# Performance work log

Hardware: AMD Instinct MI355X
Metric: run time of the kernel (lower is better)

## Reference

```python
import jax, jax.numpy as jnp
import numpy as np

E = 1024   # embed_dim
H = 512    # hidden_dim
LD = 512   # latent_dim
B = 2048   # number of users / segments
L = 48     # max segment length (pad target)


def _lrelu(x):
    return jnp.where(x > 0, x, 0.2 * x)


def setup_inputs() -> dict:
    key = jax.random.key(0)
    ks = list(jax.random.split(key, 40))
    nxt = iter(ks)

    def nrm(shape, s=1.0):
        return (jax.random.normal(next(nxt), shape, jnp.float32) * s).astype(jnp.float32)

    # ragged segment boundaries: lengths cycle {16..48}, mean 32, total 65536
    pat = np.array([16, 20, 28, 32, 32, 36, 44, 48], dtype=np.int64)
    lens = np.tile(pat, B // 8)
    starts = np.concatenate([np.zeros(1, np.int64), np.cumsum(lens)[:-1]])
    N = int(lens.sum())  # 65536
    seq_start_end = jnp.asarray(np.stack([starts, starts + lens], axis=1))

    inp = {
        'target_chosen': nrm((B, E)),
        'target_rejected': nrm((B, E)),
        'context_chosen': nrm((N, E)),
        'context_rejected': nrm((N, E)),
        'eps': nrm((B, LD)),
        # PairEncoder: 2E -> H -> H -> LD
        'pe_w1': nrm((2 * E, H), 0.02), 'pe_b1': jnp.zeros((H,), jnp.float32),
        'pe_w2': nrm((H, H), 0.02),     'pe_b2': jnp.zeros((H,), jnp.float32),
        'pe_w3': nrm((H, LD), 0.02),    'pe_b3': jnp.zeros((LD,), jnp.float32),
        # SequenceEncoder attention projections (LD -> LD)
        'wq': nrm((LD, LD), 0.02), 'bq': jnp.zeros((LD,), jnp.float32),
        'wk': nrm((LD, LD), 0.02), 'bk': jnp.zeros((LD,), jnp.float32),
        'wv': nrm((LD, LD), 0.02), 'bv': jnp.zeros((LD,), jnp.float32),
        'wm': nrm((LD, LD), 0.02), 'bm': jnp.zeros((LD,), jnp.float32),
        'wlv': nrm((LD, LD), 0.02), 'blv': jnp.zeros((LD,), jnp.float32),
        # Decoder: (E+LD) -> H -> H -> 1 (shared for chosen/rejected)
        'd_w1': nrm((E + LD, H), 0.02), 'd_b1': jnp.zeros((H,), jnp.float32),
        'd_w2': nrm((H, H), 0.02),      'd_b2': jnp.zeros((H,), jnp.float32),
        'd_w3': nrm((H, 1), 0.02),      'd_b3': jnp.zeros((1,), jnp.float32),
        'seq_start_end': seq_start_end,
        'user_type': jax.random.randint(next(nxt), (B,), 0, 4, jnp.int64),
    }
    return inp


def reference(target_chosen, target_rejected, context_chosen, context_rejected, eps,
              pe_w1, pe_b1, pe_w2, pe_b2, pe_w3, pe_b3,
              wq, bq, wk, bk, wv, bv, wm, bm, wlv, blv,
              d_w1, d_b1, d_w2, d_b2, d_w3, d_b3,
              seq_start_end, user_type):
    N = context_chosen.shape[0]

    # ---- PairEncoder: concat(chosen, rejected) -> MLP -> [N, LD] ----
    x = jnp.concatenate([context_chosen, context_rejected], axis=1)
    h = _lrelu(x @ pe_w1 + pe_b1)
    h = _lrelu(h @ pe_w2 + pe_b2)
    pair_embed = h @ pe_w3 + pe_b3  # [N, LD]

    # ---- SequenceEncoder: ragged per-segment self-attention + mean pool ----
    starts = seq_start_end[:, 0]
    lens = seq_start_end[:, 1] - starts            # [B]
    pos = jnp.arange(L)
    idx = jnp.clip(starts[:, None] + pos[None, :], 0, N - 1)   # [B, L]
    mask = pos[None, :] < lens[:, None]                        # [B, L]
    ctx = pair_embed[idx]                                      # [B, L, LD]

    q = ctx @ wq + bq
    k = ctx @ wk + bk
    v = ctx @ wv + bv
    scores = jnp.einsum('bld,bmd->blm', q, k) / jnp.float32(np.sqrt(LD))
    scores = jnp.where(mask[:, None, :], scores, jnp.float32(-1e9))
    attn = jax.nn.softmax(scores, axis=-1)
    weighted = jnp.einsum('blm,bmd->bld', attn, v)             # [B, L, LD]
    # mean over valid query rows only (matches exact-segment torch mean)
    seg_out = jnp.sum(weighted * mask[..., None], axis=1) / lens[:, None].astype(jnp.float32)

    mean = seg_out @ wm + bm
    log_var = seg_out @ wlv + blv
    mean = jnp.clip(mean, -1.0, 1.0)
    log_var = jnp.clip(log_var, -1.0, 1.0)

    # ---- reparameterization (training path) + sphere normalization ----
    z = mean + jnp.exp(0.5 * log_var) * eps
    znorm = jnp.maximum(jnp.linalg.norm(z, axis=-1, keepdims=True), 1e-12)
    z = z / znorm * jnp.float32(np.sqrt(LD))

    # ---- Decoder (shared MLP) ----
    def dec(t):
        u = jnp.concatenate([t, z], axis=1)
        u = _lrelu(u @ d_w1 + d_b1)
        u = _lrelu(u @ d_w2 + d_b2)
        return u @ d_w3 + d_b3

    rc = dec(target_chosen)
    rr = dec(target_rejected)
    return (rc, rr, mean, log_var, z)
```

## Files before the change

### kernel.cpp

```cpp
#include <hip/hip_runtime.h>
#include <stdint.h>

typedef __bf16 bf16;
typedef __attribute__((ext_vector_type(8))) __bf16 bf16x8;
typedef __attribute__((ext_vector_type(4))) float f32x4;
typedef __attribute__((ext_vector_type(4))) unsigned int u32x4;

typedef __attribute__((address_space(1))) unsigned gas_u32;
typedef __attribute__((address_space(3))) unsigned las_u32;

__device__ __forceinline__ unsigned short f2b_bits(float f) {
    unsigned u = __builtin_bit_cast(unsigned, f);
    u += 0x7fffu + ((u >> 16) & 1u);
    return (unsigned short)(u >> 16);
}
__device__ __forceinline__ bf16 f2b(float f) { return __builtin_bit_cast(bf16, f2b_bits(f)); }
__device__ __forceinline__ float lo16f(unsigned u) { return __builtin_bit_cast(float, u << 16); }
__device__ __forceinline__ float hi16f(unsigned u) { return __builtin_bit_cast(float, u & 0xffff0000u); }

__device__ __forceinline__ void gl2lds16(const void* g, void* l) {
    __builtin_amdgcn_global_load_lds((gas_u32*)(uintptr_t)g, (las_u32*)(uintptr_t)l, 16, 0, 0);
}

#define BM 128
#define BN 128
#define BK 32

template<int AMODE, int ACT, int OMODE>
__global__ __launch_bounds__(256, 2)
void gemm_k(const void* __restrict__ Ap, const void* __restrict__ Ap2,
            const bf16* __restrict__ Bt, const float* __restrict__ bias,
            void* __restrict__ Op, void* __restrict__ Op2,
            int M, int N, int K, int lda)
{
    constexpr int ASZ = (AMODE == 1) ? (BM * BK * 2) : (BM * BK);
    __shared__ __align__(16) bf16 As[ASZ];
    __shared__ __align__(16) bf16 Bs[BN * BK];
    float* Asf = (float*)As;

    const int tid  = threadIdx.x;
    const int wave = tid >> 6;
    const int lane = tid & 63;
    const int quad = lane >> 4;
    const int l16  = lane & 15;
    const int bm0 = blockIdx.y * BM;
    const int bn0 = blockIdx.x * BN;
    const int wm0 = (wave >> 1) << 6;
    const int wn0 = (wave & 1) << 6;

    f32x4 acc[4][4];
#pragma unroll
    for (int a = 0; a < 4; a++)
#pragma unroll
        for (int c = 0; c < 4; c++) acc[a][c] = {0.f, 0.f, 0.f, 0.f};

    const bf16* aptr[2];
    const float* asrc0[4];
    const float* asrc1[4];
    if constexpr (AMODE == 1) {
#pragma unroll
        for (int j = 0; j < 4; j++) {
            const int s2 = j * 256 + tid;
            const int arow = s2 >> 3, kq = s2 & 7;
            const int kgrp = kq ^ (arow & 7);
            asrc0[j] = (const float*)Ap  + (size_t)(bm0 + arow) * 1024 + kgrp * 4;
            asrc1[j] = (const float*)Ap2 + (size_t)(bm0 + arow) * 1024 + kgrp * 4;
        }
    } else {
#pragma unroll
        for (int i = 0; i < 2; i++) {
            const int s = i * 256 + tid;
            const int arow = s >> 2, kp = s & 3;
            size_t rbase;
            if constexpr (AMODE == 2) rbase = (size_t)((const int*)Ap2)[bm0 + arow] * (size_t)lda;
            else                      rbase = (size_t)(bm0 + arow) * (size_t)lda;
            aptr[i] = (const bf16*)Ap + rbase + kp * 8;
        }
    }
    const bf16* bptr[2];
#pragma unroll
    for (int i = 0; i < 2; i++) {
        const int s = i * 256 + tid;
        const int brow = s >> 2, kp = s & 3;
        bptr[i] = Bt + (size_t)(bn0 + brow) * (size_t)K + kp * 8;
    }

    for (int k0 = 0; k0 < K; k0 += BK) {
        if constexpr (AMODE == 1) {
#pragma unroll
            for (int j = 0; j < 4; j++) {
                const float* src = (k0 < 1024) ? (asrc0[j] + k0) : (asrc1[j] + (k0 - 1024));
                gl2lds16(src, &Asf[(j * 256 + (wave << 6)) * 4]);
            }
        } else {
#pragma unroll
            for (int i = 0; i < 2; i++)
                gl2lds16(aptr[i] + k0, &As[(i * 256 + (wave << 6)) * 8]);
        }
#pragma unroll
        for (int i = 0; i < 2; i++)
            gl2lds16(bptr[i] + k0, &Bs[(i * 256 + (wave << 6)) * 8]);

        __syncthreads();

        bf16x8 af[4], bfr[4];
#pragma unroll
        for (int mt = 0; mt < 4; mt++) {
            if constexpr (AMODE == 1) {
                const int r = wm0 + mt * 16 + l16;
                const int rx = r & 7;
                const f32x4 v0 = *(const f32x4*)&Asf[r * 32 + ((2 * quad) ^ rx) * 4];
                const f32x4 v1 = *(const f32x4*)&Asf[r * 32 + ((2 * quad + 1) ^ rx) * 4];
                bf16x8 t;
#pragma unroll
                for (int e = 0; e < 4; e++) { t[e] = (bf16)v0[e]; t[4 + e] = (bf16)v1[e]; }
                af[mt] = t;
            } else {
                af[mt] = *(const bf16x8*)&As[(wm0 + mt * 16 + l16) * BK + quad * 8];
            }
        }
#pragma unroll
        for (int nt = 0; nt < 4; nt++)
            bfr[nt] = *(const bf16x8*)&Bs[(wn0 + nt * 16 + l16) * BK + quad * 8];
#pragma unroll
        for (int mt = 0; mt < 4; mt++)
#pragma unroll
            for (int nt = 0; nt < 4; nt++)
                acc[mt][nt] = __builtin_amdgcn_mfma_f32_16x16x32_bf16(af[mt], bfr[nt], acc[mt][nt], 0, 0, 0);

        __syncthreads();
    }

    float bv[4];
#pragma unroll
    for (int nt = 0; nt < 4; nt++) bv[nt] = bias ? bias[bn0 + wn0 + nt * 16 + l16] : 0.f;
#pragma unroll
    for (int mt = 0; mt < 4; mt++) {
#pragma unroll
        for (int nt = 0; nt < 4; nt++) {
#pragma unroll
            for (int r = 0; r < 4; r++) {
                float v = acc[mt][nt][r] + bv[nt];
                if constexpr (ACT == 1) v = (v > 0.f) ? v : 0.2f * v;
                if constexpr (ACT == 2) v = fminf(fmaxf(v, -1.f), 1.f);
                const int row = bm0 + wm0 + mt * 16 + quad * 4 + r;
                const int col = bn0 + wn0 + nt * 16 + l16;
                if constexpr (OMODE == 0) {
                    ((bf16*)Op)[(size_t)row * N + col] = f2b(v);
                } else {
                    if (col < 512) ((float*)Op)[(size_t)row * 512 + col] = v;
                    else           ((float*)Op2)[(size_t)row * 512 + col - 512] = v;
                }
            }
        }
    }
}

struct TP8 { const float* s[8]; bf16* d[8]; };

__global__ __launch_bounds__(256)
void transpose8_k(TP8 p)
{
    __shared__ float t[64][65];
    const float* __restrict__ src = p.s[blockIdx.z];
    bf16* __restrict__ dst = p.d[blockIdx.z];
    const int tx = threadIdx.x & 63, ty = threadIdx.x >> 6;
    const int k0 = blockIdx.x * 64, n0 = blockIdx.y * 64;
#pragma unroll
    for (int j = 0; j < 16; j++) {
        const int r = j * 4 + ty;
        t[r][tx] = src[(size_t)(k0 + r) * 512 + n0 + tx];
    }
    __syncthreads();
#pragma unroll
    for (int j = 0; j < 16; j++) {
        const int r = j * 4 + ty;
        dst[(size_t)(n0 + r) * 512 + k0 + tx] = f2b(t[tx][r]);
    }
}

__global__ __launch_bounds__(256)
void transpose_g_k(const float* __restrict__ src, bf16* __restrict__ dst, int K)
{
    __shared__ float t[64][65];
    const int tx = threadIdx.x & 63, ty = threadIdx.x >> 6;
    const int k0 = blockIdx.x * 64, n0 = blockIdx.y * 64;
#pragma unroll
    for (int j = 0; j < 16; j++) {
        const int r = j * 4 + ty;
        t[r][tx] = src[(size_t)(k0 + r) * 512 + n0 + tx];
    }
    __syncthreads();
#pragma unroll
    for (int j = 0; j < 16; j++) {
        const int r = j * 4 + ty;
        dst[(size_t)(n0 + r) * K + k0 + tx] = f2b(t[tx][r]);
    }
}

__global__ void prep_misc_k(const float* bq, const float* bk, const float* bv,
                            const float* bm, const float* blv,
                            float* bqkv, float* bml,
                            const int* sse, int* rowidx, int Nctx)
{
    const int i = blockIdx.x * 256 + threadIdx.x;
    if (i < 512) {
        bqkv[i] = bq[i]; bqkv[512 + i] = bk[i]; bqkv[1024 + i] = bv[i];
        bml[i] = bm[i];  bml[512 + i] = blv[i];
    }
    if (i < 98304) {
        const int b = i / 48, l = i - b * 48;
        int s = sse[2 * b] + l;
        s = (s < 0) ? 0 : ((s >= Nctx) ? (Nctx - 1) : s);
        rowidx[i] = s;
    }
}

__global__ __launch_bounds__(256, 2)
void attn_k(const bf16* __restrict__ qkv, const int* __restrict__ sse, bf16* __restrict__ seg)
{
    __shared__ bf16 qsh[48 * 128];
    __shared__ bf16 ksh[48 * 128];
    __shared__ float ss[48 * 49];
    __shared__ float wbuf[4 * 48];
    __shared__ float wfin[48];

    const int b = blockIdx.x;
    const int tid = threadIdx.x;
    const int wave = tid >> 6, lane = tid & 63;
    const int len = sse[2 * b + 1] - sse[2 * b];
    const size_t rowbase = (size_t)b * (48 * 1536);

    int pl[9], pm[9]; float sc[9];
    const int np = len * len;
#pragma unroll
    for (int i = 0; i < 9; i++) {
        const int p = tid + i * 256;
        if (p < np) { pl[i] = p / len; pm[i] = p - pl[i] * len; }
        else pl[i] = -1;
        sc[i] = 0.f;
    }

    int srow[3], scol[3];
#pragma unroll
    for (int j = 0; j < 3; j++) { const int t = j * 256 + tid; srow[j] = t >> 4; scol[j] = t & 15; }

    for (int ch = 0; ch < 4; ch++) {
#pragma unroll
        for (int j = 0; j < 3; j++) {
            const int row = srow[j], c = scol[j];
            const bf16* g = qkv + rowbase + (size_t)row * 1536 + (ch << 7) + (c << 3);
            const int lc = row * 128 + ((c ^ (row & 15)) << 3);
            *(bf16x8*)&qsh[lc] = *(const bf16x8*)g;
            *(bf16x8*)&ksh[lc] = *(const bf16x8*)(g + 512);
        }
        __syncthreads();
#pragma unroll
        for (int i = 0; i < 9; i++) {
            if (pl[i] < 0) continue;
            const int l = pl[i], m = pm[i];
            const int lbase = l * 128, mbase = m * 128;
            const int lx = l & 15, mx = m & 15;
            float s0 = 0.f, s1 = 0.f;
#pragma unroll 1
            for (int c8 = 0; c8 < 16; c8++) {
                const bf16x8 qv = *(const bf16x8*)&qsh[lbase + ((c8 ^ lx) << 3)];
                const bf16x8 kv = *(const bf16x8*)&ksh[mbase + ((c8 ^ mx) << 3)];
                const u32x4 qu = __builtin_bit_cast(u32x4, qv);
                const u32x4 ku = __builtin_bit_cast(u32x4, kv);
#pragma unroll
                for (int t = 0; t < 4; t++) {
                    s0 += lo16f(qu[t]) * lo16f(ku[t]);
                    s1 += hi16f(qu[t]) * hi16f(ku[t]);
                }
            }
            sc[i] += s0 + s1;
        }
        __syncthreads();
    }

#pragma unroll
    for (int i = 0; i < 9; i++)
        if (pl[i] >= 0) ss[pl[i] * 49 + pm[i]] = sc[i] * 0.044194173824159216f;
    __syncthreads();

    float wacc = 0.f;
    for (int l = wave; l < len; l += 4) {
        const float v = (lane < len) ? ss[l * 49 + lane] : -3.0e38f;
        float mx = v;
#pragma unroll
        for (int o = 32; o; o >>= 1) mx = fmaxf(mx, __shfl_xor(mx, o));
        const float e = (lane < len) ? __expf(v - mx) : 0.f;
        float sm = e;
#pragma unroll
        for (int o = 32; o; o >>= 1) sm += __shfl_xor(sm, o);
        wacc += e / sm;
    }
    if (lane < 48) wbuf[wave * 48 + lane] = wacc;
    __syncthreads();
    if (tid < 48) wfin[tid] = wbuf[tid] + wbuf[48 + tid] + wbuf[96 + tid] + wbuf[144 + tid];
    __syncthreads();

    const int d0 = tid * 2;
    float a0 = 0.f, a1 = 0.f;
    for (int m = 0; m < len; m++) {
        const float wv = wfin[m];
        const unsigned u = *(const unsigned*)(qkv + rowbase + (size_t)m * 1536 + 1024 + d0);
        a0 += wv * lo16f(u);
        a1 += wv * hi16f(u);
    }
    const float inv = 1.f / (float)len;
    seg[(size_t)b * 512 + d0]     = f2b(a0 * inv);
    seg[(size_t)b * 512 + d0 + 1] = f2b(a1 * inv);
}

__global__ __launch_bounds__(256)
void z_k(const float* __restrict__ meanp, const float* __restrict__ lvp,
         const float* __restrict__ eps, const float* __restrict__ tc, const float* __restrict__ tr,
         float* __restrict__ zoutp, bf16* __restrict__ U)
{
    __shared__ float red[4];
    const int b = blockIdx.x, tid = threadIdx.x;
    const int wave = tid >> 6, lane = tid & 63;
    const int d0 = tid * 2;
    float z0[2];
#pragma unroll
    for (int j = 0; j < 2; j++) {
        const float m = meanp[(size_t)b * 512 + d0 + j];
        const float l = lvp[(size_t)b * 512 + d0 + j];
        const float e = eps[(size_t)b * 512 + d0 + j];
        z0[j] = m + __expf(0.5f * l) * e;
    }
    float ssum = z0[0] * z0[0] + z0[1] * z0[1];
#pragma unroll
    for (int o = 32; o; o >>= 1) ssum += __shfl_xor(ssum, o);
    if (lane == 0) red[wave] = ssum;
    __syncthreads();
    const float tot = red[0] + red[1] + red[2] + red[3];
    float nrm = fmaxf(sqrtf(tot), 1e-12f);
    const float s = 22.627416997969522f / nrm;
#pragma unroll
    for (int j = 0; j < 2; j++) {
        const float z = z0[j] * s;
        zoutp[(size_t)b * 512 + d0 + j] = z;
        const bf16 zb = f2b(z);
        U[(size_t)b * 1536 + 1024 + d0 + j] = zb;
        U[(size_t)(2048 + b) * 1536 + 1024 + d0 + j] = zb;
    }
#pragma unroll
    for (int j = 0; j < 4; j++) {
        const int d = tid + j * 256;
        U[(size_t)b * 1536 + d]          = f2b(tc[(size_t)b * 1024 + d]);
        U[(size_t)(2048 + b) * 1536 + d] = f2b(tr[(size_t)b * 1024 + d]);
    }
}

__global__ __launch_bounds__(256)
void dec3_k(const bf16* __restrict__ D2, const float* __restrict__ w3, const float* __restrict__ b3,
            float* __restrict__ out)
{
    const int gw = (blockIdx.x * 256 + threadIdx.x) >> 6;
    const int lane = threadIdx.x & 63;
    const bf16x8 d = *(const bf16x8*)(D2 + (size_t)gw * 512 + lane * 8);
    const u32x4 du = __builtin_bit_cast(u32x4, d);
    float s = 0.f;
#pragma unroll
    for (int t = 0; t < 4; t++) {
        s += lo16f(du[t]) * w3[lane * 8 + 2 * t];
        s += hi16f(du[t]) * w3[lane * 8 + 2 * t + 1];
    }
#pragma unroll
    for (int o = 32; o; o >>= 1) s += __shfl_xor(s, o);
    if (lane == 0) out[gw] = s + b3[0];
}

extern "C" void kernel_launch(void* const* d_in, const int* in_sizes, int n_in,
                              void* d_out, int out_size, void* d_ws, size_t ws_size,
                              hipStream_t stream)
{
    const float* tc    = (const float*)d_in[0];
    const float* tr    = (const float*)d_in[1];
    const float* cc    = (const float*)d_in[2];
    const float* cr    = (const float*)d_in[3];
    const float* eps   = (const float*)d_in[4];
    const float* pe_w1 = (const float*)d_in[5];
    const float* pe_b1 = (const float*)d_in[6];
    const float* pe_w2 = (const float*)d_in[7];
    const float* pe_b2 = (const float*)d_in[8];
    const float* pe_w3 = (const float*)d_in[9];
    const float* pe_b3 = (const float*)d_in[10];
    const float* wq    = (const float*)d_in[11];
    const float* bq    = (const float*)d_in[12];
    const float* wk    = (const float*)d_in[13];
    const float* bk    = (const float*)d_in[14];
    const float* wv    = (const float*)d_in[15];
    const float* bv    = (const float*)d_in[16];
    const float* wm    = (const float*)d_in[17];
    const float* bm    = (const float*)d_in[18];
    const float* wlv   = (const float*)d_in[19];
    const float* blv   = (const float*)d_in[20];
    const float* d_w1  = (const float*)d_in[21];
    const float* d_b1  = (const float*)d_in[22];
    const float* d_w2  = (const float*)d_in[23];
    const float* d_b2  = (const float*)d_in[24];
    const float* d_w3  = (const float*)d_in[25];
    const float* d_b3  = (const float*)d_in[26];
    const int*   sse   = (const int*)d_in[27];
    const int Nctx = in_sizes[2] / 1024;

    uint8_t* wsp = (uint8_t*)d_ws;
    size_t off = 0;
    auto alloc = [&](size_t bytes) -> void* {
        void* p = wsp + off;
        off += (bytes + 255) & ~(size_t)255;
        return p;
    };

    bf16* pe_w1t = (bf16*)alloc((size_t)2048 * 512 * 2);
    bf16* pe_w2t = (bf16*)alloc((size_t)512 * 512 * 2);
    bf16* pe_w3t = (bf16*)alloc((size_t)512 * 512 * 2);
    bf16* wqkvt  = (bf16*)alloc((size_t)1536 * 512 * 2);
    bf16* wmlt   = (bf16*)alloc((size_t)1024 * 512 * 2);
    bf16* d_w1t  = (bf16*)alloc((size_t)512 * 1536 * 2);
    bf16* d_w2t  = (bf16*)alloc((size_t)512 * 512 * 2);
    float* bqkv  = (float*)alloc(1536 * 4);
    float* bml   = (float*)alloc(1024 * 4);
    int* rowidx  = (int*)alloc((size_t)98304 * 4);
    bf16* seg    = (bf16*)alloc((size_t)2048 * 512 * 2);
    bf16* U      = (bf16*)alloc((size_t)4096 * 1536 * 2);
    bf16* D1     = (bf16*)alloc((size_t)4096 * 512 * 2);
    bf16* D2     = (bf16*)alloc((size_t)4096 * 512 * 2);
    bf16* hbuf   = (bf16*)alloc((size_t)Nctx * 512 * 2);
    bf16* bigbuf = (bf16*)alloc((size_t)98304 * 1536 * 2);
    bf16* h1  = hbuf;
    bf16* h2  = bigbuf;
    bf16* peb = hbuf;
    bf16* qkv = bigbuf;

    float* outp  = (float*)d_out;
    float* meanp = outp + 4096;
    float* lvp   = outp + 4096 + 2048 * 512;
    float* zoutp = outp + 4096 + 2 * 2048 * 512;

    TP8 tp;
    tp.s[0] = pe_w2; tp.d[0] = pe_w2t;
    tp.s[1] = pe_w3; tp.d[1] = pe_w3t;
    tp.s[2] = wq;    tp.d[2] = wqkvt;
    tp.s[3] = wk;    tp.d[3] = wqkvt + 512 * 512;
    tp.s[4] = wv;    tp.d[4] = wqkvt + 1024 * 512;
    tp.s[5] = wm;    tp.d[5] = wmlt;
    tp.s[6] = wlv;   tp.d[6] = wmlt + 512 * 512;
    tp.s[7] = d_w2;  tp.d[7] = d_w2t;
    transpose8_k<<<dim3(8, 8, 8), 256, 0, stream>>>(tp);
    transpose_g_k<<<dim3(32, 8), 256, 0, stream>>>(pe_w1, pe_w1t, 2048);
    transpose_g_k<<<dim3(24, 8), 256, 0, stream>>>(d_w1, d_w1t, 1536);
    prep_misc_k<<<384, 256, 0, stream>>>(bq, bk, bv, bm, blv, bqkv, bml, sse, rowidx, Nctx);

    gemm_k<1, 1, 0><<<dim3(4, Nctx / 128), 256, 0, stream>>>(cc, cr, pe_w1t, pe_b1, h1, nullptr, Nctx, 512, 2048, 1024);
    gemm_k<0, 1, 0><<<dim3(4, Nctx / 128), 256, 0, stream>>>(h1, nullptr, pe_w2t, pe_b2, h2, nullptr, Nctx, 512, 512, 512);
    gemm_k<0, 0, 0><<<dim3(4, Nctx / 128), 256, 0, stream>>>(h2, nullptr, pe_w3t, pe_b3, peb, nullptr, Nctx, 512, 512, 512);

    gemm_k<2, 0, 0><<<dim3(12, 768), 256, 0, stream>>>(peb, rowidx, wqkvt, bqkv, qkv, nullptr, 98304, 1536, 512, 512);

    attn_k<<<2048, 256, 0, stream>>>(qkv, sse, seg);

    gemm_k<0, 2, 1><<<dim3(8, 16), 256, 0, stream>>>(seg, nullptr, wmlt, bml, meanp, lvp, 2048, 1024, 512, 512);

    z_k<<<2048, 256, 0, stream>>>(meanp, lvp, eps, tc, tr, zoutp, U);

    gemm_k<0, 1, 0><<<dim3(4, 32), 256, 0, stream>>>(U, nullptr, d_w1t, d_b1, D1, nullptr, 4096, 512, 1536, 1536);
    gemm_k<0, 1, 0><<<dim3(4, 32), 256, 0, stream>>>(D1, nullptr, d_w2t, d_b2, D2, nullptr, 4096, 512, 512, 512);
    dec3_k<<<1024, 256, 0, stream>>>(D2, d_w3, d_b3, outp);

    (void)n_in; (void)out_size; (void)ws_size; (void)in_sizes;
}
```

Baseline: 1.389 ms.

## Compute QKV on packed rows and prefetch fp32 A tile via registers

```diff
diff --git a/kernel.cpp b/kernel.cpp
--- a/kernel.cpp
+++ b/kernel.cpp
@@ -33,10 +33,8 @@
             void* __restrict__ Op, void* __restrict__ Op2,
             int M, int N, int K, int lda)
 {
-    constexpr int ASZ = (AMODE == 1) ? (BM * BK * 2) : (BM * BK);
-    __shared__ __align__(16) bf16 As[ASZ];
+    __shared__ __align__(16) bf16 As[BM * BK];
     __shared__ __align__(16) bf16 Bs[BN * BK];
-    float* Asf = (float*)As;
 
     const int tid  = threadIdx.x;
     const int wave = tid >> 6;
@@ -55,17 +53,14 @@
         for (int c = 0; c < 4; c++) acc[a][c] = {0.f, 0.f, 0.f, 0.f};
 
     const bf16* aptr[2];
-    const float* asrc0[4];
-    const float* asrc1[4];
+    const float* a0base = nullptr;
+    const float* a1base = nullptr;
+    f32x4 areg[4];
     if constexpr (AMODE == 1) {
-#pragma unroll
-        for (int j = 0; j < 4; j++) {
-            const int s2 = j * 256 + tid;
-            const int arow = s2 >> 3, kq = s2 & 7;
-            const int kgrp = kq ^ (arow & 7);
-            asrc0[j] = (const float*)Ap  + (size_t)(bm0 + arow) * 1024 + kgrp * 4;
-            asrc1[j] = (const float*)Ap2 + (size_t)(bm0 + arow) * 1024 + kgrp * 4;
-        }
+        a0base = (const float*)Ap  + (size_t)(bm0 + (tid >> 1)) * 1024 + (tid & 1) * 16;
+        a1base = (const float*)Ap2 + (size_t)(bm0 + (tid >> 1)) * 1024 + (tid & 1) * 16;
+#pragma unroll
+        for (int j = 0; j < 4; j++) areg[j] = *(const f32x4*)(a0base + j * 4);
     } else {
 #pragma unroll
         for (int i = 0; i < 2; i++) {
@@ -86,39 +81,38 @@
     }
 
     for (int k0 = 0; k0 < K; k0 += BK) {
+#pragma unroll
+        for (int i = 0; i < 2; i++)
+            gl2lds16(bptr[i] + k0, &Bs[(i * 256 + (wave << 6)) * 8]);
+
         if constexpr (AMODE == 1) {
-#pragma unroll
-            for (int j = 0; j < 4; j++) {
-                const float* src = (k0 < 1024) ? (asrc0[j] + k0) : (asrc1[j] + (k0 - 1024));
-                gl2lds16(src, &Asf[(j * 256 + (wave << 6)) * 4]);
+            bf16x8 w0, w1;
+#pragma unroll
+            for (int e = 0; e < 4; e++) {
+                w0[e]     = (bf16)areg[0][e];
+                w0[4 + e] = (bf16)areg[1][e];
+                w1[e]     = (bf16)areg[2][e];
+                w1[4 + e] = (bf16)areg[3][e];
             }
+            bf16* dst = &As[(tid >> 1) * BK + (tid & 1) * 16];
+            *(bf16x8*)dst       = w0;
+            *(bf16x8*)(dst + 8) = w1;
+            const int kn = (k0 + BK < K) ? (k0 + BK) : 0;
+            const float* s = (kn < 1024) ? (a0base + kn) : (a1base + (kn - 1024));
+#pragma unroll
+            for (int j = 0; j < 4; j++) areg[j] = *(const f32x4*)(s + j * 4);
         } else {
 #pragma unroll
             for (int i = 0; i < 2; i++)
                 gl2lds16(aptr[i] + k0, &As[(i * 256 + (wave << 6)) * 8]);
         }
-#pragma unroll
-        for (int i = 0; i < 2; i++)
-            gl2lds16(bptr[i] + k0, &Bs[(i * 256 + (wave << 6)) * 8]);
 
         __syncthreads();
 
         bf16x8 af[4], bfr[4];
 #pragma unroll
-        for (int mt = 0; mt < 4; mt++) {
-            if constexpr (AMODE == 1) {
-                const int r = wm0 + mt * 16 + l16;
-                const int rx = r & 7;
-                const f32x4 v0 = *(const f32x4*)&Asf[r * 32 + ((2 * quad) ^ rx) * 4];
-                const f32x4 v1 = *(const f32x4*)&Asf[r * 32 + ((2 * quad + 1) ^ rx) * 4];
-                bf16x8 t;
-#pragma unroll
-                for (int e = 0; e < 4; e++) { t[e] = (bf16)v0[e]; t[4 + e] = (bf16)v1[e]; }
-                af[mt] = t;
-            } else {
-                af[mt] = *(const bf16x8*)&As[(wm0 + mt * 16 + l16) * BK + quad * 8];
-            }
-        }
+        for (int mt = 0; mt < 4; mt++)
+            af[mt] = *(const bf16x8*)&As[(wm0 + mt * 16 + l16) * BK + quad * 8];
 #pragma unroll
         for (int nt = 0; nt < 4; nt++)
             bfr[nt] = *(const bf16x8*)&Bs[(wn0 + nt * 16 + l16) * BK + quad * 8];
@@ -200,19 +194,12 @@
 
 __global__ void prep_misc_k(const float* bq, const float* bk, const float* bv,
                             const float* bm, const float* blv,
-                            float* bqkv, float* bml,
-                            const int* sse, int* rowidx, int Nctx)
+                            float* bqkv, float* bml)
 {
     const int i = blockIdx.x * 256 + threadIdx.x;
     if (i < 512) {
         bqkv[i] = bq[i]; bqkv[512 + i] = bk[i]; bqkv[1024 + i] = bv[i];
         bml[i] = bm[i];  bml[512 + i] = blv[i];
-    }
-    if (i < 98304) {
-        const int b = i / 48, l = i - b * 48;
-        int s = sse[2 * b] + l;
-        s = (s < 0) ? 0 : ((s >= Nctx) ? (Nctx - 1) : s);
-        rowidx[i] = s;
     }
 }
 
@@ -228,8 +215,9 @@
     const int b = blockIdx.x;
     const int tid = threadIdx.x;
     const int wave = tid >> 6, lane = tid & 63;
-    const int len = sse[2 * b + 1] - sse[2 * b];
-    const size_t rowbase = (size_t)b * (48 * 1536);
+    const int st  = sse[2 * b];
+    const int len = sse[2 * b + 1] - st;
+    const size_t rowbase = (size_t)st * 1536;
 
     int pl[9], pm[9]; float sc[9];
     const int np = len * len;
@@ -425,13 +413,12 @@
     bf16* d_w2t  = (bf16*)alloc((size_t)512 * 512 * 2);
     float* bqkv  = (float*)alloc(1536 * 4);
     float* bml   = (float*)alloc(1024 * 4);
-    int* rowidx  = (int*)alloc((size_t)98304 * 4);
     bf16* seg    = (bf16*)alloc((size_t)2048 * 512 * 2);
     bf16* U      = (bf16*)alloc((size_t)4096 * 1536 * 2);
     bf16* D1     = (bf16*)alloc((size_t)4096 * 512 * 2);
     bf16* D2     = (bf16*)alloc((size_t)4096 * 512 * 2);
     bf16* hbuf   = (bf16*)alloc((size_t)Nctx * 512 * 2);
-    bf16* bigbuf = (bf16*)alloc((size_t)98304 * 1536 * 2);
+    bf16* bigbuf = (bf16*)alloc((size_t)Nctx * 1536 * 2);
     bf16* h1  = hbuf;
     bf16* h2  = bigbuf;
     bf16* peb = hbuf;
@@ -454,13 +441,13 @@
     transpose8_k<<<dim3(8, 8, 8), 256, 0, stream>>>(tp);
     transpose_g_k<<<dim3(32, 8), 256, 0, stream>>>(pe_w1, pe_w1t, 2048);
     transpose_g_k<<<dim3(24, 8), 256, 0, stream>>>(d_w1, d_w1t, 1536);
-    prep_misc_k<<<384, 256, 0, stream>>>(bq, bk, bv, bm, blv, bqkv, bml, sse, rowidx, Nctx);
+    prep_misc_k<<<2, 256, 0, stream>>>(bq, bk, bv, bm, blv, bqkv, bml);
 
     gemm_k<1, 1, 0><<<dim3(4, Nctx / 128), 256, 0, stream>>>(cc, cr, pe_w1t, pe_b1, h1, nullptr, Nctx, 512, 2048, 1024);
     gemm_k<0, 1, 0><<<dim3(4, Nctx / 128), 256, 0, stream>>>(h1, nullptr, pe_w2t, pe_b2, h2, nullptr, Nctx, 512, 512, 512);
     gemm_k<0, 0, 0><<<dim3(4, Nctx / 128), 256, 0, stream>>>(h2, nullptr, pe_w3t, pe_b3, peb, nullptr, Nctx, 512, 512, 512);
 
-    gemm_k<2, 0, 0><<<dim3(12, 768), 256, 0, stream>>>(peb, rowidx, wqkvt, bqkv, qkv, nullptr, 98304, 1536, 512, 512);
+    gemm_k<0, 0, 0><<<dim3(12, Nctx / 128), 256, 0, stream>>>(peb, nullptr, wqkvt, bqkv, qkv, nullptr, Nctx, 1536, 512, 512);
 
     attn_k<<<2048, 256, 0, stream>>>(qkv, sse, seg);
 
```

Measured after the change: 1.338 ms. -3.6%, faster.
